# Kernel optimization log

Hardware: AMD Instinct MI355X
Metric: run time of the kernel (lower is better)

Reference implementation:

```python
import jax, jax.numpy as jnp
import numpy as np

N, E, DIN, DL, DOUT, G, K = 50000, 800000, 32, 128, 10, 256, 3


def setup_inputs() -> dict:
    key = jax.random.key(0)
    ks = jax.random.split(key, 24)
    rn = lambda k, s: jax.random.normal(k, s, jnp.float32) * 0.05
    inp = {}
    inp["x"] = jax.random.normal(ks[0], (N, DIN), jnp.float32)
    inp["edge_index"] = jax.random.randint(ks[1], (2, E), 0, N, jnp.int32)
    inp["batch_ids"] = jnp.sort(jax.random.randint(ks[2], (N,), 0, G, jnp.int32))
    inp["y"] = jax.random.uniform(ks[3], (G, DOUT), dtype=jnp.float32)
    inp["eps"] = jax.random.uniform(ks[4], (K, N, DL), dtype=jnp.float32)  # torch.rand_like -> uniform
    inp["W_in"] = rn(ks[5], (DIN, DL)); inp["b_in"] = jnp.zeros((DL,), jnp.float32)
    inp["W_gcn"] = rn(ks[6], (DL, DL)); inp["b_gcn"] = jnp.zeros((DL,), jnp.float32)
    inp["W_enc"] = rn(ks[7], (5, DL, DL)); inp["b_enc"] = jnp.zeros((5, DL), jnp.float32)
    inp["W_mu"] = rn(ks[8], (DL, DL)); inp["b_mu"] = jnp.zeros((DL,), jnp.float32)
    inp["W_std"] = rn(ks[9], (DL, DL)); inp["b_std"] = jnp.zeros((DL,), jnp.float32)
    dims = [DL, 256, 128, 64, 32, 16]
    for i in range(5):
        inp[f"Wd{i}"] = rn(ks[10 + i], (dims[i], dims[i + 1]))
        inp[f"bd{i}"] = jnp.zeros((dims[i + 1],), jnp.float32)
    inp["Wo"] = rn(ks[15], (16, DOUT)); inp["bo"] = jnp.zeros((DOUT,), jnp.float32)
    inp["k"] = K
    return inp


def reference(x, edge_index, batch_ids, y, eps, W_in, b_in, W_gcn, b_gcn,
              W_enc, b_enc, W_mu, b_mu, W_std, b_std,
              Wd0, bd0, Wd1, bd1, Wd2, bd2, Wd3, bd3, Wd4, bd4, Wo, bo, k):
    n = x.shape[0]
    src, dst = edge_index[0], edge_index[1]
    # GCN symmetric normalization with self-loops (PyG gcn_norm, edge_weight=1)
    deg = jnp.zeros((n,), x.dtype).at[dst].add(1.0) + 1.0  # +1 for self-loop
    dinv = jax.lax.rsqrt(deg)
    enorm = (dinv[src] * dinv[dst])[:, None]  # [E,1]
    snorm = (dinv * dinv)[:, None]            # [N,1] self-loop norm

    h = jax.nn.sigmoid(x @ W_in + b_in)  # input layer
    mu = h; std = h
    for i in range(k):  # k hops of MPEncoder (shared weights)
        g = h @ W_gcn  # [N,DL]
        g = jax.ops.segment_sum(g[src] * enorm, dst, num_segments=n) + g * snorm + b_gcn
        for j in range(5):
            g = jax.nn.sigmoid(g @ W_enc[j] + b_enc[j])
        mu = g @ W_mu + b_mu
        std = jax.nn.softplus(g @ W_std + b_std - 5.0)
        h = mu + std * eps[i]  # reparametrization with uniform noise

    # Decoder MLP per node, sigmoid output
    d = h
    for Wd, bd in ((Wd0, bd0), (Wd1, bd1), (Wd2, bd2), (Wd3, bd3), (Wd4, bd4)):
        d = jax.nn.relu(d @ Wd + bd)
    yp = jax.nn.sigmoid(d @ Wo + bo)  # [N,DOUT]

    # global_mean_pool over graphs
    g_count = y.shape[0]
    sums = jax.ops.segment_sum(yp, batch_ids, num_segments=g_count)
    cnt = jax.ops.segment_sum(jnp.ones((n,), yp.dtype), batch_ids, num_segments=g_count)
    y_pred = sums / jnp.maximum(cnt, 1.0)[:, None]
    return (y_pred, mu, std, y)
```

## Files before the change

### kernel.cpp

```cpp
#include <hip/hip_runtime.h>
#include <math.h>

#define DIN 32
#define DL 128
#define DOUT 10

typedef _Float16 f16x8 __attribute__((ext_vector_type(8)));
typedef float f32x4 __attribute__((ext_vector_type(4)));

__device__ __forceinline__ float sigm(float x){ return 1.0f/(1.0f+expf(-x)); }
__device__ __forceinline__ float softplus_(float x){ return fmaxf(x,0.0f) + log1pf(expf(-fabsf(x))); }

__global__ void count_edges_k(const int* __restrict__ ei, int* __restrict__ cnt, int E){
    int e = blockIdx.x*256 + threadIdx.x;
    if (e < E) atomicAdd(&cnt[ei[E + e]], 1);
}

__global__ void dinv_k(const int* __restrict__ cnt, float* __restrict__ dinv, int N){
    int i = blockIdx.x*256 + threadIdx.x;
    if (i < N) dinv[i] = rsqrtf((float)cnt[i] + 1.0f);
}

__global__ void block_sum_k(const int* __restrict__ cnt, int* __restrict__ bsum, int n){
    __shared__ int ws_[4];
    int tid = threadIdx.x;
    int i = blockIdx.x*256 + tid;
    int v = (i < n) ? cnt[i] : 0;
    #pragma unroll
    for (int off = 32; off > 0; off >>= 1) v += __shfl_xor(v, off);
    if ((tid & 63) == 0) ws_[tid >> 6] = v;
    __syncthreads();
    if (tid == 0) bsum[blockIdx.x] = ws_[0] + ws_[1] + ws_[2] + ws_[3];
}

__global__ void scan_bsum_k(int* __restrict__ bsum, int nb){
    __shared__ int tmp[1024];
    int tid = threadIdx.x;
    int v = (tid < nb) ? bsum[tid] : 0;
    tmp[tid] = v; __syncthreads();
    for (int off = 1; off < 1024; off <<= 1){
        int t = (tid >= off) ? tmp[tid-off] : 0;
        __syncthreads();
        tmp[tid] += t;
        __syncthreads();
    }
    if (tid < nb) bsum[tid] = tmp[tid] - v;
}

__global__ void block_scan_k(const int* __restrict__ cnt, const int* __restrict__ bexcl,
                             int* __restrict__ cursor, int* __restrict__ rowptr, int n){
    __shared__ int tmp[256];
    int tid = threadIdx.x;
    int i = blockIdx.x*256 + tid;
    int v = (i < n) ? cnt[i] : 0;
    tmp[tid] = v; __syncthreads();
    for (int off = 1; off < 256; off <<= 1){
        int t = (tid >= off) ? tmp[tid-off] : 0;
        __syncthreads();
        tmp[tid] += t;
        __syncthreads();
    }
    int excl = bexcl[blockIdx.x] + tmp[tid] - v;
    if (i < n){ cursor[i] = excl; rowptr[i+1] = excl + v; }
    if (i == 0) rowptr[0] = 0;
}

__global__ void place_edges_k(const int* __restrict__ ei, int* __restrict__ cursor,
                              int* __restrict__ csr_src, int E){
    int e = blockIdx.x*256 + threadIdx.x;
    if (e < E){
        int s = ei[e], d = ei[E + e];
        csr_src[atomicAdd(&cursor[d], 1)] = s;
    }
}

struct WPA { const float* s; _Float16* d; int K; int C; };
struct WPA14 { WPA a[14]; };
__global__ void wprep_all_k(WPA14 args){
    WPA w = args.a[blockIdx.y];
    int idx = blockIdx.x*256 + threadIdx.x;
    if (idx < w.K*w.C){ int k = idx / w.C, c = idx % w.C; w.d[(size_t)c*w.K + k] = (_Float16)w.s[idx]; }
}

template<int K, int NC16, bool ZERO>
__device__ __forceinline__ void mfma_ldsmm(const _Float16* As, int lda,
        const _Float16* Ws, int ldw, f32x4 (&acc)[2][8], int ln, int q, int wid){
    if (ZERO){
        #pragma unroll
        for (int r = 0; r < 2; ++r)
            #pragma unroll
            for (int c = 0; c < 8; ++c) acc[r][c] = (f32x4){0.f,0.f,0.f,0.f};
    }
    #pragma unroll
    for (int kk = 0; kk < K/32; ++kk){
        int ko = kk*32 + q*8;
        f16x8 a0 = *(const f16x8*)&As[(size_t)(wid*32 + ln)*lda + ko];
        f16x8 a1 = *(const f16x8*)&As[(size_t)(wid*32 + 16 + ln)*lda + ko];
        #pragma unroll
        for (int c = 0; c < NC16; ++c){
            f16x8 b = *(const f16x8*)&Ws[(size_t)(c*16 + ln)*ldw + ko];
            acc[0][c] = __builtin_amdgcn_mfma_f32_16x16x32_f16(a0, b, acc[0][c], 0, 0, 0);
            acc[1][c] = __builtin_amdgcn_mfma_f32_16x16x32_f16(a1, b, acc[1][c], 0, 0, 0);
        }
    }
}

template<int NC16, int ACT>
__device__ __forceinline__ void act_store_lds(_Float16* D, int ldd, f32x4 (&acc)[2][8],
        const float* bias, int ln, int q, int wid){
    #pragma unroll
    for (int r = 0; r < 2; ++r){
        int rowb = wid*32 + r*16 + q*4;
        #pragma unroll
        for (int c = 0; c < NC16; ++c){
            int col = c*16 + ln;
            float bv = bias ? bias[col] : 0.0f;
            #pragma unroll
            for (int i2 = 0; i2 < 4; ++i2){
                float v = acc[r][c][i2] + bv;
                if (ACT == 1) v = sigm(v);
                else if (ACT == 2) v = fmaxf(v, 0.0f);
                D[(size_t)(rowb + i2)*ldd + col] = (_Float16)v;
            }
        }
    }
}

__device__ __forceinline__ void stage_w(const _Float16* Wg, _Float16* Wl, int ldw,
                                        int C, int K, int tid){
    int kq = K/8, tot = C*kq;
    for (int i = tid; i < tot; i += 256){
        int r = i/kq, s = i%kq;
        *(f16x8*)&Wl[(size_t)r*ldw + s*8] = *(const f16x8*)&Wg[(size_t)r*K + s*8];
    }
}

__global__ __launch_bounds__(256,1) void fused_input_k(const float* __restrict__ x,
        const _Float16* __restrict__ WtIN, const float* __restrict__ b_in,
        const _Float16* __restrict__ WtGCN, _Float16* __restrict__ gOut, int nrows){
    __shared__ __align__(16) _Float16 Ax[128*40];
    __shared__ __align__(16) _Float16 Hl[128*136];
    __shared__ __align__(16) _Float16 Wi[128*40];
    __shared__ __align__(16) _Float16 Wg[128*136];
    int tid = threadIdx.x, lane = tid & 63, wid = tid >> 6;
    int ln = lane & 15, q = lane >> 4;
    int row0 = blockIdx.x * 128;
    for (int i = tid; i < 512; i += 256){
        int r = i >> 2, s = i & 3;
        f16x8 v = {};
        if (row0 + r < nrows){
            const float* xs = &x[(size_t)(row0+r)*DIN + s*8];
            float4 u0 = *(const float4*)xs, u1 = *(const float4*)(xs+4);
            v[0]=(_Float16)u0.x; v[1]=(_Float16)u0.y; v[2]=(_Float16)u0.z; v[3]=(_Float16)u0.w;
            v[4]=(_Float16)u1.x; v[5]=(_Float16)u1.y; v[6]=(_Float16)u1.z; v[7]=(_Float16)u1.w;
        }
        *(f16x8*)&Ax[r*40 + s*8] = v;
        *(f16x8*)&Wi[r*40 + s*8] = *(const f16x8*)&WtIN[(size_t)r*32 + s*8];
    }
    for (int i = tid; i < 2048; i += 256){
        int r = i >> 4, s = i & 15;
        *(f16x8*)&Wg[r*136 + s*8] = *(const f16x8*)&WtGCN[(size_t)r*128 + s*8];
    }
    __syncthreads();
    f32x4 acc[2][8];
    mfma_ldsmm<32,8,true>(Ax, 40, Wi, 40, acc, ln, q, wid);
    act_store_lds<8,1>(Hl, 136, acc, b_in, ln, q, wid);
    __syncthreads();
    mfma_ldsmm<128,8,true>(Hl, 136, Wg, 136, acc, ln, q, wid);
    #pragma unroll
    for (int r = 0; r < 2; ++r){
        int rowb = row0 + wid*32 + r*16 + q*4;
        #pragma unroll
        for (int c = 0; c < 8; ++c){
            int col = c*16 + ln;
            #pragma unroll
            for (int i2 = 0; i2 < 4; ++i2){
                int row = rowb + i2;
                if (row < nrows) gOut[(size_t)row*DL + col] = (_Float16)acc[r][c][i2];
            }
        }
    }
}

__global__ __launch_bounds__(256) void gcn_agg_h(const _Float16* __restrict__ g,
        _Float16* __restrict__ out, const int* __restrict__ rowptr,
        const int* __restrict__ csr_src, const float* __restrict__ dinv,
        const float* __restrict__ bgcn, int N){
    int t = threadIdx.x;
    int node = blockIdx.x*16 + (t >> 4);
    int f = (t & 15)*8;
    if (node >= N) return;
    float dv = dinv[node];
    float sn = dv*dv;
    f16x8 sv = *(const f16x8*)&g[(size_t)node*DL + f];
    float acc[8];
    #pragma unroll
    for (int j = 0; j < 8; ++j) acc[j] = (float)sv[j]*sn + bgcn[f+j];
    int e = rowptr[node], e1 = rowptr[node+1];
    for (; e + 4 <= e1; e += 4){
        int s0 = csr_src[e], s1 = csr_src[e+1], s2 = csr_src[e+2], s3 = csr_src[e+3];
        float w0 = dinv[s0]*dv, w1 = dinv[s1]*dv, w2 = dinv[s2]*dv, w3 = dinv[s3]*dv;
        f16x8 n0 = *(const f16x8*)&g[(size_t)s0*DL + f];
        f16x8 n1 = *(const f16x8*)&g[(size_t)s1*DL + f];
        f16x8 n2 = *(const f16x8*)&g[(size_t)s2*DL + f];
        f16x8 n3 = *(const f16x8*)&g[(size_t)s3*DL + f];
        #pragma unroll
        for (int j = 0; j < 8; ++j)
            acc[j] += (float)n0[j]*w0 + (float)n1[j]*w1 + (float)n2[j]*w2 + (float)n3[j]*w3;
    }
    for (; e < e1; ++e){
        int s = csr_src[e];
        float w = dinv[s]*dv;
        f16x8 nv = *(const f16x8*)&g[(size_t)s*DL + f];
        #pragma unroll
        for (int j = 0; j < 8; ++j) acc[j] += (float)nv[j]*w;
    }
    f16x8 o;
    #pragma unroll
    for (int j = 0; j < 8; ++j) o[j] = (_Float16)acc[j];
    *(f16x8*)&out[(size_t)node*DL + f] = o;
}

template<int LAST>
__global__ __launch_bounds__(256,2) void hop2_k(const _Float16* __restrict__ g2,
        const _Float16* __restrict__ Wt8, const float* __restrict__ b_enc,
        const float* __restrict__ b_mu, const float* __restrict__ b_std,
        const float* __restrict__ eps_i, _Float16* __restrict__ gOut,
        float* __restrict__ muOut, float* __restrict__ stdOut,
        _Float16* __restrict__ hOut, int nrows){
    __shared__ __align__(16) _Float16 Act[128*136];
    __shared__ __align__(16) _Float16 Wb[128*136];
    int tid = threadIdx.x, lane = tid & 63, wid = tid >> 6;
    int ln = lane & 15, q = lane >> 4;
    int row0 = blockIdx.x * 128;
    for (int i = tid; i < 2048; i += 256){
        int r = i >> 4, s = i & 15;
        f16x8 v = {};
        if (row0 + r < nrows) v = *(const f16x8*)&g2[(size_t)(row0+r)*DL + s*8];
        *(f16x8*)&Act[r*136 + s*8] = v;
    }
    f32x4 acc[2][8];
    auto stageW = [&](int m){
        __syncthreads();
        stage_w(Wt8 + (size_t)m*16384, Wb, 136, 128, 128, tid);
        __syncthreads();
    };
    #pragma unroll 1
    for (int j = 0; j < 5; ++j){
        stageW(1+j);
        mfma_ldsmm<128,8,true>(Act, 136, Wb, 136, acc, ln, q, wid);
        act_store_lds<8,1>(Act, 136, acc, b_enc + j*DL, ln, q, wid);
    }
    stageW(7);
    mfma_ldsmm<128,8,true>(Act, 136, Wb, 136, acc, ln, q, wid);
    f16x8 se[2][4];
    #pragma unroll
    for (int r = 0; r < 2; ++r){
        int rowb = row0 + wid*32 + r*16 + q*4;
        #pragma unroll
        for (int c = 0; c < 8; ++c){
            int col = c*16 + ln;
            float bs = b_std[col];
            #pragma unroll
            for (int i2 = 0; i2 < 4; ++i2){
                int grow = rowb + i2;
                float s = softplus_(acc[r][c][i2] + bs - 5.0f);
                float ev = (grow < nrows) ? eps_i[(size_t)grow*DL + col] : 0.0f;
                int fi = c*4 + i2;
                se[r][fi>>3][fi&7] = (_Float16)(s*ev);
                if (LAST && grow < nrows) stdOut[(size_t)grow*DL + col] = s;
            }
        }
    }
    stageW(6);
    mfma_ldsmm<128,8,true>(Act, 136, Wb, 136, acc, ln, q, wid);
    #pragma unroll
    for (int r = 0; r < 2; ++r){
        int rowl = wid*32 + r*16 + q*4;
        #pragma unroll
        for (int c = 0; c < 8; ++c){
            int col = c*16 + ln;
            float bm = b_mu[col];
            #pragma unroll
            for (int i2 = 0; i2 < 4; ++i2){
                int grow = row0 + rowl + i2;
                float mv = acc[r][c][i2] + bm;
                int fi = c*4 + i2;
                float hv = mv + (float)se[r][fi>>3][fi&7];
                Act[(size_t)(rowl + i2)*136 + col] = (_Float16)hv;
                if (LAST && grow < nrows){
                    muOut[(size_t)grow*DL + col] = mv;
                    hOut[(size_t)grow*DL + col] = (_Float16)hv;
                }
            }
        }
    }
    if (!LAST){
        stageW(0);
        mfma_ldsmm<128,8,true>(Act, 136, Wb, 136, acc, ln, q, wid);
        #pragma unroll
        for (int r = 0; r < 2; ++r){
            int rowb = row0 + wid*32 + r*16 + q*4;
            #pragma unroll
            for (int c = 0; c < 8; ++c){
                int col = c*16 + ln;
                #pragma unroll
                for (int i2 = 0; i2 < 4; ++i2){
                    int grow = rowb + i2;
                    if (grow < nrows) gOut[(size_t)grow*DL + col] = (_Float16)acc[r][c][i2];
                }
            }
        }
    }
}

__global__ __launch_bounds__(256,1) void decoder_k(const _Float16* __restrict__ h,
        const _Float16* __restrict__ WtD0, const _Float16* __restrict__ WtD1,
        const _Float16* __restrict__ WtD2, const _Float16* __restrict__ WtD3,
        const _Float16* __restrict__ WtD4,
        const float* __restrict__ bd0, const float* __restrict__ bd1,
        const float* __restrict__ bd2, const float* __restrict__ bd3,
        const float* __restrict__ bd4, const float* __restrict__ Wo,
        const float* __restrict__ bo, const int* __restrict__ batch,
        float* __restrict__ sums, float* __restrict__ gcnt, int nrows){
    __shared__ __align__(16) _Float16 A[128*136];
    __shared__ __align__(16) _Float16 B[128*264];
    __shared__ __align__(16) _Float16 W[128*136];
    __shared__ float WoL[16*DOUT];
    __shared__ float boL[DOUT];
    int tid = threadIdx.x, lane = tid & 63, wid = tid >> 6;
    int ln = lane & 15, q = lane >> 4;
    int row0 = blockIdx.x * 128;
    for (int i = tid; i < 2048; i += 256){
        int r = i >> 4, s = i & 15;
        f16x8 v = {};
        if (row0 + r < nrows) v = *(const f16x8*)&h[(size_t)(row0+r)*DL + s*8];
        *(f16x8*)&A[r*136 + s*8] = v;
    }
    if (tid < 16*DOUT) WoL[tid] = Wo[tid];
    if (tid < DOUT) boL[tid] = bo[tid];
    f32x4 acc[2][8];
    for (int ch = 0; ch < 2; ++ch){
        stage_w(WtD0 + (size_t)ch*128*128, W, 136, 128, 128, tid);
        __syncthreads();
        mfma_ldsmm<128,8,true>(A, 136, W, 136, acc, ln, q, wid);
        act_store_lds<8,2>(B + ch*128, 264, acc, bd0 + ch*128, ln, q, wid);
        __syncthreads();
    }
    for (int kh = 0; kh < 2; ++kh){
        for (int i = tid; i < 2048; i += 256){
            int r = i >> 4, s = i & 15;
            *(f16x8*)&W[r*136 + s*8] = *(const f16x8*)&WtD1[(size_t)r*256 + kh*128 + s*8];
        }
        __syncthreads();
        if (kh == 0) mfma_ldsmm<128,8,true >(B,       264, W, 136, acc, ln, q, wid);
        else         mfma_ldsmm<128,8,false>(B + 128, 264, W, 136, acc, ln, q, wid);
        __syncthreads();
    }
    act_store_lds<8,2>(A, 136, acc, bd1, ln, q, wid);
    __syncthreads();
    stage_w(WtD2, W, 136, 64, 128, tid);
    __syncthreads();
    mfma_ldsmm<128,4,true>(A, 136, W, 136, acc, ln, q, wid);
    act_store_lds<4,2>(B, 264, acc, bd2, ln, q, wid);
    __syncthreads();
    stage_w(WtD3, W, 136, 32, 64, tid);
    __syncthreads();
    mfma_ldsmm<64,2,true>(B, 264, W, 136, acc, ln, q, wid);
    act_store_lds<2,2>(A, 136, acc, bd3, ln, q, wid);
    __syncthreads();
    stage_w(WtD4, W, 136, 16, 32, tid);
    __syncthreads();
    mfma_ldsmm<32,1,true>(A, 136, W, 136, acc, ln, q, wid);
    act_store_lds<1,2>(B, 264, acc, bd4, ln, q, wid);
    __syncthreads();
    int node = row0 + tid;
    bool valid = (tid < 128) && (node < nrows);
    float yp[DOUT];
    int b = -1;
    if (valid){
        float dd[16];
        #pragma unroll
        for (int k = 0; k < 16; ++k) dd[k] = (float)B[(size_t)tid*264 + k];
        #pragma unroll
        for (int o = 0; o < DOUT; ++o){
            float a2 = boL[o];
            #pragma unroll
            for (int k = 0; k < 16; ++k) a2 += dd[k]*WoL[k*DOUT + o];
            yp[o] = sigm(a2);
        }
        b = batch[node];
    }
    int b0 = __builtin_amdgcn_readfirstlane(b);
    unsigned long long m = __ballot(b == b0);
    if (m == ~0ull && b0 >= 0){
        #pragma unroll
        for (int o = 0; o < DOUT; ++o){
            float v = yp[o];
            for (int off = 32; off > 0; off >>= 1) v += __shfl_xor(v, off);
            if ((tid & 63) == 0) atomicAdd(&sums[b0*DOUT + o], v);
        }
        if ((tid & 63) == 0) atomicAdd(&gcnt[b0], 64.0f);
    } else if (valid){
        #pragma unroll
        for (int o = 0; o < DOUT; ++o) atomicAdd(&sums[b*DOUT + o], yp[o]);
        atomicAdd(&gcnt[b], 1.0f);
    }
}

__global__ void divide_k(float* __restrict__ out, const float* __restrict__ gcnt, int n){
    int i = blockIdx.x*256 + threadIdx.x;
    if (i < n) out[i] = out[i] / fmaxf(gcnt[i/DOUT], 1.0f);
}

__global__ void copy_k(const float* __restrict__ src, float* __restrict__ dst, int n){
    int i = blockIdx.x*256 + threadIdx.x;
    if (i < n) dst[i] = src[i];
}

extern "C" void kernel_launch(void* const* d_in, const int* in_sizes, int n_in,
                              void* d_out, int out_size, void* d_ws, size_t ws_size,
                              hipStream_t stream) {
    const float* x     = (const float*)d_in[0];
    const int*   ei    = (const int*)d_in[1];
    const int*   batch = (const int*)d_in[2];
    const float* y     = (const float*)d_in[3];
    const float* eps   = (const float*)d_in[4];
    const float* W_in  = (const float*)d_in[5];
    const float* b_in  = (const float*)d_in[6];
    const float* W_gcn = (const float*)d_in[7];
    const float* b_gcn = (const float*)d_in[8];
    const float* W_enc = (const float*)d_in[9];
    const float* b_enc = (const float*)d_in[10];
    const float* W_mu  = (const float*)d_in[11];
    const float* b_mu  = (const float*)d_in[12];
    const float* W_std = (const float*)d_in[13];
    const float* b_std = (const float*)d_in[14];
    const float* Wd0 = (const float*)d_in[15]; const float* bd0 = (const float*)d_in[16];
    const float* Wd1 = (const float*)d_in[17]; const float* bd1 = (const float*)d_in[18];
    const float* Wd2 = (const float*)d_in[19]; const float* bd2 = (const float*)d_in[20];
    const float* Wd3 = (const float*)d_in[21]; const float* bd3 = (const float*)d_in[22];
    const float* Wd4 = (const float*)d_in[23]; const float* bd4 = (const float*)d_in[24];
    const float* Wo  = (const float*)d_in[25]; const float* bo  = (const float*)d_in[26];

    const int N = in_sizes[2];
    const int E = in_sizes[1]/2;
    const int G = in_sizes[3]/DOUT;
    const int KHOP = in_sizes[4] / (N*DL);
    const size_t NN = (size_t)N*DL;

    char* p = (char*)d_ws;
    auto take = [&p](size_t bytes) -> char* {
        char* r = p; p += (bytes + 255) & ~(size_t)255; return r;
    };
    _Float16* hG  = (_Float16*)take(NN*2);
    _Float16* hG2 = (_Float16*)take(NN*2);
    _Float16* hH  = (_Float16*)take(NN*2);
    float* dinv  = (float*)take((size_t)N*4);
    float* gcnt  = (float*)take((size_t)G*4);
    int* cnt     = (int*)take((size_t)N*4);
    int* rowptr  = (int*)take((size_t)(N+1)*4);
    int* cursor  = (int*)take((size_t)N*4);
    int* csr_src = (int*)take((size_t)E*4);
    int* bsum    = (int*)take(1024*4);
    _Float16* Wt8  = (_Float16*)take((size_t)8*DL*DL*2);
    _Float16* WtIN = (_Float16*)take((size_t)DL*DIN*2);
    _Float16* WtD0 = (_Float16*)take((size_t)256*128*2);
    _Float16* WtD1 = (_Float16*)take((size_t)128*256*2);
    _Float16* WtD2 = (_Float16*)take((size_t)64*128*2);
    _Float16* WtD3 = (_Float16*)take((size_t)32*64*2);
    _Float16* WtD4 = (_Float16*)take((size_t)16*32*2);

    float* out_ypred = (float*)d_out;
    float* out_mu    = out_ypred + (size_t)G*DOUT;
    float* out_std   = out_mu + NN;
    float* out_y     = out_std + NN;

    hipMemsetAsync(cnt, 0, sizeof(int)*N, stream);
    hipMemsetAsync(out_ypred, 0, sizeof(float)*G*DOUT, stream);
    hipMemsetAsync(gcnt, 0, sizeof(float)*G, stream);

    int gE = (E + 255)/256, gN = (N + 255)/256;
    int nb = gN;

    count_edges_k<<<gE, 256, 0, stream>>>(ei, cnt, E);
    dinv_k<<<gN, 256, 0, stream>>>(cnt, dinv, N);
    block_sum_k<<<nb, 256, 0, stream>>>(cnt, bsum, N);
    scan_bsum_k<<<1, 1024, 0, stream>>>(bsum, nb);
    block_scan_k<<<nb, 256, 0, stream>>>(cnt, bsum, cursor, rowptr, N);
    place_edges_k<<<gE, 256, 0, stream>>>(ei, cursor, csr_src, E);

    WPA14 wa;
    wa.a[0]  = { W_in,  WtIN, DIN, DL };
    wa.a[1]  = { W_gcn, Wt8,  DL, DL };
    for (int j = 0; j < 5; ++j) wa.a[2+j] = { W_enc + (size_t)j*DL*DL, Wt8 + (size_t)(1+j)*DL*DL, DL, DL };
    wa.a[7]  = { W_mu,  Wt8 + (size_t)6*DL*DL, DL, DL };
    wa.a[8]  = { W_std, Wt8 + (size_t)7*DL*DL, DL, DL };
    wa.a[9]  = { Wd0, WtD0, 128, 256 };
    wa.a[10] = { Wd1, WtD1, 256, 128 };
    wa.a[11] = { Wd2, WtD2, 128, 64 };
    wa.a[12] = { Wd3, WtD3, 64, 32 };
    wa.a[13] = { Wd4, WtD4, 32, 16 };
    wprep_all_k<<<dim3(128, 14), 256, 0, stream>>>(wa);

    int ntile = (N + 127)/128;
    fused_input_k<<<ntile, 256, 0, stream>>>(x, WtIN, b_in, Wt8, hG, N);

    for (int i = 0; i < KHOP; ++i){
        gcn_agg_h<<<(N+15)/16, 256, 0, stream>>>(hG, hG2, rowptr, csr_src, dinv, b_gcn, N);
        const float* eps_i = eps + (size_t)i*NN;
        if (i == KHOP-1)
            hop2_k<1><<<ntile, 256, 0, stream>>>(hG2, Wt8, b_enc, b_mu, b_std, eps_i,
                                                 nullptr, out_mu, out_std, hH, N);
        else
            hop2_k<0><<<ntile, 256, 0, stream>>>(hG2, Wt8, b_enc, b_mu, b_std, eps_i,
                                                 hG, nullptr, nullptr, nullptr, N);
    }

    decoder_k<<<ntile, 256, 0, stream>>>(hH, WtD0, WtD1, WtD2, WtD3, WtD4,
                                         bd0, bd1, bd2, bd3, bd4, Wo, bo,
                                         batch, out_ypred, gcnt, N);
    divide_k<<<(G*DOUT+255)/256, 256, 0, stream>>>(out_ypred, gcnt, G*DOUT);
    copy_k<<<(G*DOUT+255)/256, 256, 0, stream>>>(y, out_y, G*DOUT);
}
```

Baseline: 793.5 us.

## Prefetch hop weights into registers during MFMA; shrink decoder tile to 64 rows

In hop2_k, the next weight matrix is now loaded from global memory into registers while the current MFMA runs, then written to LDS after a barrier. This hides weight-staging latency and removes one barrier per stage. The decoder moves to 64-row tiles with smaller LDS buffers and interleaves the Wd0 and Wd1 chunks, so two blocks can fit per CU and occupancy rises. The cost is extra register pressure from the prefetch buffers and twice as many decoder blocks, each staging the same weights.

```diff
diff --git a/kernel.cpp b/kernel.cpp
--- a/kernel.cpp
+++ b/kernel.cpp
@@ -126,12 +126,57 @@
     }
 }
 
-__device__ __forceinline__ void stage_w(const _Float16* Wg, _Float16* Wl, int ldw,
-                                        int C, int K, int tid){
+template<int K, int NC16, bool ZERO>
+__device__ __forceinline__ void gemm64(const _Float16* As, const _Float16* Ws,
+        f32x4 (&acc)[NC16], int ln, int q, int wid){
+    if (ZERO){
+        #pragma unroll
+        for (int c = 0; c < NC16; ++c) acc[c] = (f32x4){0.f,0.f,0.f,0.f};
+    }
+    #pragma unroll
+    for (int kk = 0; kk < K/32; ++kk){
+        int ko = kk*32 + q*8;
+        f16x8 a = *(const f16x8*)&As[(size_t)(wid*16 + ln)*136 + ko];
+        #pragma unroll
+        for (int c = 0; c < NC16; ++c){
+            f16x8 b = *(const f16x8*)&Ws[(size_t)(c*16 + ln)*136 + ko];
+            acc[c] = __builtin_amdgcn_mfma_f32_16x16x32_f16(a, b, acc[c], 0, 0, 0);
+        }
+    }
+}
+
+template<int NC16>
+__device__ __forceinline__ void relu_st64(_Float16* D, f32x4 (&acc)[NC16],
+        const float* bias, int ln, int q, int wid){
+    int rowb = wid*16 + q*4;
+    #pragma unroll
+    for (int c = 0; c < NC16; ++c){
+        int col = c*16 + ln;
+        float bv = bias[col];
+        #pragma unroll
+        for (int i2 = 0; i2 < 4; ++i2)
+            D[(size_t)(rowb + i2)*136 + col] = (_Float16)fmaxf(acc[c][i2] + bv, 0.0f);
+    }
+}
+
+__device__ __forceinline__ void stage_w2(const _Float16* Wg, int srcStride, int kOff,
+                                         int C, int K, _Float16* Wl, int tid){
     int kq = K/8, tot = C*kq;
     for (int i = tid; i < tot; i += 256){
         int r = i/kq, s = i%kq;
-        *(f16x8*)&Wl[(size_t)r*ldw + s*8] = *(const f16x8*)&Wg[(size_t)r*K + s*8];
+        *(f16x8*)&Wl[(size_t)r*136 + s*8] = *(const f16x8*)&Wg[(size_t)r*srcStride + kOff + s*8];
+    }
+}
+
+__device__ __forceinline__ void pf_load_w(const _Float16* Wg, f16x8 (&pf)[8], int tid){
+    #pragma unroll
+    for (int i = 0; i < 8; ++i) pf[i] = *(const f16x8*)&Wg[(size_t)(tid + i*256)*8];
+}
+__device__ __forceinline__ void pf_store_w(_Float16* Wl, f16x8 (&pf)[8], int tid){
+    #pragma unroll
+    for (int i = 0; i < 8; ++i){
+        int g = tid + i*256; int r = g >> 4, s = g & 15;
+        *(f16x8*)&Wl[(size_t)r*136 + s*8] = pf[i];
     }
 }
 
@@ -233,26 +278,30 @@
     int tid = threadIdx.x, lane = tid & 63, wid = tid >> 6;
     int ln = lane & 15, q = lane >> 4;
     int row0 = blockIdx.x * 128;
+    f16x8 pf[8];
+    pf_load_w(Wt8 + (size_t)1*16384, pf, tid);
     for (int i = tid; i < 2048; i += 256){
         int r = i >> 4, s = i & 15;
         f16x8 v = {};
         if (row0 + r < nrows) v = *(const f16x8*)&g2[(size_t)(row0+r)*DL + s*8];
         *(f16x8*)&Act[r*136 + s*8] = v;
     }
+    pf_store_w(Wb, pf, tid);
+    __syncthreads();
     f32x4 acc[2][8];
-    auto stageW = [&](int m){
-        __syncthreads();
-        stage_w(Wt8 + (size_t)m*16384, Wb, 136, 128, 128, tid);
-        __syncthreads();
-    };
     #pragma unroll 1
     for (int j = 0; j < 5; ++j){
-        stageW(1+j);
+        pf_load_w(Wt8 + (size_t)((j < 4) ? (2+j) : 7)*16384, pf, tid);
         mfma_ldsmm<128,8,true>(Act, 136, Wb, 136, acc, ln, q, wid);
+        __syncthreads();
+        pf_store_w(Wb, pf, tid);
         act_store_lds<8,1>(Act, 136, acc, b_enc + j*DL, ln, q, wid);
-    }
-    stageW(7);
+        __syncthreads();
+    }
+    pf_load_w(Wt8 + (size_t)6*16384, pf, tid);
     mfma_ldsmm<128,8,true>(Act, 136, Wb, 136, acc, ln, q, wid);
+    __syncthreads();
+    pf_store_w(Wb, pf, tid);
     f16x8 se[2][4];
     #pragma unroll
     for (int r = 0; r < 2; ++r){
@@ -272,31 +321,48 @@
             }
         }
     }
-    stageW(6);
+    __syncthreads();
+    if (!LAST) pf_load_w(Wt8, pf, tid);
     mfma_ldsmm<128,8,true>(Act, 136, Wb, 136, acc, ln, q, wid);
-    #pragma unroll
-    for (int r = 0; r < 2; ++r){
-        int rowl = wid*32 + r*16 + q*4;
-        #pragma unroll
-        for (int c = 0; c < 8; ++c){
-            int col = c*16 + ln;
-            float bm = b_mu[col];
-            #pragma unroll
-            for (int i2 = 0; i2 < 4; ++i2){
-                int grow = row0 + rowl + i2;
-                float mv = acc[r][c][i2] + bm;
-                int fi = c*4 + i2;
-                float hv = mv + (float)se[r][fi>>3][fi&7];
-                Act[(size_t)(rowl + i2)*136 + col] = (_Float16)hv;
-                if (LAST && grow < nrows){
-                    muOut[(size_t)grow*DL + col] = mv;
-                    hOut[(size_t)grow*DL + col] = (_Float16)hv;
+    if (LAST){
+        #pragma unroll
+        for (int r = 0; r < 2; ++r){
+            int rowb = row0 + wid*32 + r*16 + q*4;
+            #pragma unroll
+            for (int c = 0; c < 8; ++c){
+                int col = c*16 + ln;
+                float bm = b_mu[col];
+                #pragma unroll
+                for (int i2 = 0; i2 < 4; ++i2){
+                    int grow = rowb + i2;
+                    if (grow < nrows){
+                        float mv = acc[r][c][i2] + bm;
+                        int fi = c*4 + i2;
+                        muOut[(size_t)grow*DL + col] = mv;
+                        hOut[(size_t)grow*DL + col] = (_Float16)(mv + (float)se[r][fi>>3][fi&7]);
+                    }
                 }
             }
         }
-    }
-    if (!LAST){
-        stageW(0);
+    } else {
+        __syncthreads();
+        pf_store_w(Wb, pf, tid);
+        #pragma unroll
+        for (int r = 0; r < 2; ++r){
+            int rowl = wid*32 + r*16 + q*4;
+            #pragma unroll
+            for (int c = 0; c < 8; ++c){
+                int col = c*16 + ln;
+                float bm = b_mu[col];
+                #pragma unroll
+                for (int i2 = 0; i2 < 4; ++i2){
+                    int fi = c*4 + i2;
+                    float hv = acc[r][c][i2] + bm + (float)se[r][fi>>3][fi&7];
+                    Act[(size_t)(rowl + i2)*136 + col] = (_Float16)hv;
+                }
+            }
+        }
+        __syncthreads();
         mfma_ldsmm<128,8,true>(Act, 136, Wb, 136, acc, ln, q, wid);
         #pragma unroll
         for (int r = 0; r < 2; ++r){
@@ -314,7 +380,7 @@
     }
 }
 
-__global__ __launch_bounds__(256,1) void decoder_k(const _Float16* __restrict__ h,
+__global__ __launch_bounds__(256,2) void decoder_k(const _Float16* __restrict__ h,
         const _Float16* __restrict__ WtD0, const _Float16* __restrict__ WtD1,
         const _Float16* __restrict__ WtD2, const _Float16* __restrict__ WtD3,
         const _Float16* __restrict__ WtD4,
@@ -323,15 +389,15 @@
         const float* __restrict__ bd4, const float* __restrict__ Wo,
         const float* __restrict__ bo, const int* __restrict__ batch,
         float* __restrict__ sums, float* __restrict__ gcnt, int nrows){
-    __shared__ __align__(16) _Float16 A[128*136];
-    __shared__ __align__(16) _Float16 B[128*264];
+    __shared__ __align__(16) _Float16 A[64*136];
+    __shared__ __align__(16) _Float16 B[64*136];
     __shared__ __align__(16) _Float16 W[128*136];
     __shared__ float WoL[16*DOUT];
     __shared__ float boL[DOUT];
     int tid = threadIdx.x, lane = tid & 63, wid = tid >> 6;
     int ln = lane & 15, q = lane >> 4;
-    int row0 = blockIdx.x * 128;
-    for (int i = tid; i < 2048; i += 256){
+    int row0 = blockIdx.x * 64;
+    for (int i = tid; i < 1024; i += 256){
         int r = i >> 4, s = i & 15;
         f16x8 v = {};
         if (row0 + r < nrows) v = *(const f16x8*)&h[(size_t)(row0+r)*DL + s*8];
@@ -339,49 +405,45 @@
     }
     if (tid < 16*DOUT) WoL[tid] = Wo[tid];
     if (tid < DOUT) boL[tid] = bo[tid];
-    f32x4 acc[2][8];
+    f32x4 acc0[8], acc1[8];
+    #pragma unroll 1
     for (int ch = 0; ch < 2; ++ch){
-        stage_w(WtD0 + (size_t)ch*128*128, W, 136, 128, 128, tid);
-        __syncthreads();
-        mfma_ldsmm<128,8,true>(A, 136, W, 136, acc, ln, q, wid);
-        act_store_lds<8,2>(B + ch*128, 264, acc, bd0 + ch*128, ln, q, wid);
-        __syncthreads();
-    }
-    for (int kh = 0; kh < 2; ++kh){
-        for (int i = tid; i < 2048; i += 256){
-            int r = i >> 4, s = i & 15;
-            *(f16x8*)&W[r*136 + s*8] = *(const f16x8*)&WtD1[(size_t)r*256 + kh*128 + s*8];
-        }
-        __syncthreads();
-        if (kh == 0) mfma_ldsmm<128,8,true >(B,       264, W, 136, acc, ln, q, wid);
-        else         mfma_ldsmm<128,8,false>(B + 128, 264, W, 136, acc, ln, q, wid);
-        __syncthreads();
-    }
-    act_store_lds<8,2>(A, 136, acc, bd1, ln, q, wid);
-    __syncthreads();
-    stage_w(WtD2, W, 136, 64, 128, tid);
-    __syncthreads();
-    mfma_ldsmm<128,4,true>(A, 136, W, 136, acc, ln, q, wid);
-    act_store_lds<4,2>(B, 264, acc, bd2, ln, q, wid);
-    __syncthreads();
-    stage_w(WtD3, W, 136, 32, 64, tid);
-    __syncthreads();
-    mfma_ldsmm<64,2,true>(B, 264, W, 136, acc, ln, q, wid);
-    act_store_lds<2,2>(A, 136, acc, bd3, ln, q, wid);
-    __syncthreads();
-    stage_w(WtD4, W, 136, 16, 32, tid);
-    __syncthreads();
-    mfma_ldsmm<32,1,true>(A, 136, W, 136, acc, ln, q, wid);
-    act_store_lds<1,2>(B, 264, acc, bd4, ln, q, wid);
+        if (ch) __syncthreads();
+        stage_w2(WtD0 + (size_t)ch*128*128, 128, 0, 128, 128, W, tid);
+        __syncthreads();
+        gemm64<128,8,true>(A, W, acc0, ln, q, wid);
+        relu_st64<8>(B, acc0, bd0 + ch*128, ln, q, wid);
+        __syncthreads();
+        stage_w2(WtD1, 256, ch*128, 128, 128, W, tid);
+        __syncthreads();
+        if (ch == 0) gemm64<128,8,true >(B, W, acc1, ln, q, wid);
+        else         gemm64<128,8,false>(B, W, acc1, ln, q, wid);
+    }
+    relu_st64<8>(A, acc1, bd1, ln, q, wid);
+    __syncthreads();
+    stage_w2(WtD2, 128, 0, 64, 128, W, tid);
+    __syncthreads();
+    gemm64<128,4,true>(A, W, *(f32x4(*)[4])acc0, ln, q, wid);
+    relu_st64<4>(B, *(f32x4(*)[4])acc0, bd2, ln, q, wid);
+    __syncthreads();
+    stage_w2(WtD3, 64, 0, 32, 64, W, tid);
+    __syncthreads();
+    gemm64<64,2,true>(B, W, *(f32x4(*)[2])acc0, ln, q, wid);
+    relu_st64<2>(A, *(f32x4(*)[2])acc0, bd3, ln, q, wid);
+    __syncthreads();
+    stage_w2(WtD4, 32, 0, 16, 32, W, tid);
+    __syncthreads();
+    gemm64<32,1,true>(A, W, *(f32x4(*)[1])acc0, ln, q, wid);
+    relu_st64<1>(B, *(f32x4(*)[1])acc0, bd4, ln, q, wid);
     __syncthreads();
     int node = row0 + tid;
-    bool valid = (tid < 128) && (node < nrows);
+    bool valid = (tid < 64) && (node < nrows);
     float yp[DOUT];
     int b = -1;
     if (valid){
         float dd[16];
         #pragma unroll
-        for (int k = 0; k < 16; ++k) dd[k] = (float)B[(size_t)tid*264 + k];
+        for (int k = 0; k < 16; ++k) dd[k] = (float)B[(size_t)tid*136 + k];
         #pragma unroll
         for (int o = 0; o < DOUT; ++o){
             float a2 = boL[o];
@@ -517,9 +579,9 @@
                                                  hG, nullptr, nullptr, nullptr, N);
     }
 
-    decoder_k<<<ntile, 256, 0, stream>>>(hH, WtD0, WtD1, WtD2, WtD3, WtD4,
-                                         bd0, bd1, bd2, bd3, bd4, Wo, bo,
-                                         batch, out_ypred, gcnt, N);
+    decoder_k<<<(N+63)/64, 256, 0, stream>>>(hH, WtD0, WtD1, WtD2, WtD3, WtD4,
+                                             bd0, bd1, bd2, bd3, bd4, Wo, bo,
+                                             batch, out_ypred, gcnt, N);
     divide_k<<<(G*DOUT+255)/256, 256, 0, stream>>>(out_ypred, gcnt, G*DOUT);
     copy_k<<<(G*DOUT+255)/256, 256, 0, stream>>>(y, out_y, G*DOUT);
 }
```

After: 776.3 us. -2.2%, faster.
